# Optimization experiments

Measured on AMD Instinct MI355X. Metric: run time of the kernel, lower is better.

## Reference

```python
import jax, jax.numpy as jnp
import numpy as np

N_TH1 = 30
LB = 1e-20
UB = 1e20
LB_EXP = -20.0
UB_EXP = 20.0


def make_directions(n_th1):
    # Reproduces the TF __init__ direction sampling on the sphere.
    n_th2 = 2 * (n_th1 - 1) + 1
    th1 = np.linspace(-np.pi / 2, np.pi / 2, n_th1)
    th2 = np.linspace(-np.pi, np.pi, n_th2)
    c1, s1 = np.cos(th1), np.sin(th1)
    c2, s2 = np.cos(th2), np.sin(th2)
    dx = np.outer(c1[1:-1], c2[:-1])          # [n_th1-2, n_th2-1]
    dy = np.outer(c1[1:-1], s2[:-1])
    dz = np.broadcast_to(s1[1:-1, None], dx.shape)
    mid = np.stack([dx, dy, dz], -1).reshape(-1, 3)
    poles = np.array([[c1[0] * c2[0], c1[0] * s2[0], s1[0]],
                      [c1[-1] * c2[0], c1[-1] * s2[0], s1[-1]]])
    return np.concatenate([mid, poles], 0).astype(np.float32)  # [D, 3]


def setup_inputs() -> dict:
    key = jax.random.key(0)
    k1, k2, k3 = jax.random.split(key, 3)
    vertices = jax.random.normal(k1, (8, 64, 32, 3), jnp.float32)
    # smoothness is a p-norm exponent; realistic range [2, 20]
    smoothness = 2.0 + 18.0 * jax.random.uniform(k2, (8, 64), jnp.float32)
    pointcloud = jax.random.normal(k3, (8, 2048, 3), jnp.float32)
    return {"vertices": vertices, "smoothness": smoothness, "pointcloud": pointcloud}


def _spt_forward(vertices, smoothness):
    dirs = jnp.asarray(make_directions(N_TH1))            # [D, 3]
    B, P = vertices.shape[0], vertices.shape[1]
    mean_v = jnp.mean(vertices, axis=2, keepdims=True)    # [B,P,1,3]
    local_v = vertices - mean_v                           # [B,P,V,3]

    # z = <v, x> for every vertex/direction pair -> [B,P,V,D]
    z = jnp.einsum('bpvc,dc->bpvd', local_v, dirs)
    zm = jnp.maximum(z, 0.0)
    p = smoothness[:, :, None, None]                      # [B,P,1,1]

    # dynamic rescaling k = 10^ceil(...) to keep zm^p in fp range
    zm_max = jnp.max(zm, axis=2, keepdims=True)           # [B,P,1,D]
    zm_log = jnp.log(zm_max) / jnp.log(10.0)              # = max over V of log10(zm)
    exponent = zm_log * p
    lk = jnp.where(exponent < LB_EXP, (-15.0 - exponent) / p, 0.0)
    k = 10.0 ** jnp.clip(jnp.ceil(lk), 0.0, UB_EXP)       # [B,P,1,D]
    k = jax.lax.stop_gradient(k)                          # ceil has zero grad anyway

    zm = zm * k
    pos = zm > 0
    # clip(zm^p, lb, ub) - (zm==0)*lb  ==  where(zm>0, clip(zm^p,lb,ub), 0)
    zm_p = jnp.where(pos, jnp.clip(jnp.where(pos, zm, 1.0) ** p, LB, UB), 0.0)
    sum_zm_p = jnp.sum(zm_p, axis=2, keepdims=True)       # [B,P,1,D]
    spos = sum_zm_p > 0
    h = jnp.where(spos, jnp.clip(jnp.where(spos, sum_zm_p, 1.0) ** (1.0 / p), LB, UB), LB)

    # dh/dz = clip((zm/h)^(p-1), lb, ub)
    ratio = zm / h                                        # [B,P,V,D]
    rpos = ratio > 0
    dhdz = jnp.where(rpos, jnp.clip(jnp.where(rpos, ratio, 1.0) ** (p - 1.0), LB, UB), LB)
    # dh/dx = dhdz^T @ vertices -> surface points
    dhdx = jnp.einsum('bpvd,bpvc->bpdc', dhdz, local_v)   # [B,P,D,3]
    surf = dhdx + mean_v                                  # broadcast [B,P,1,3]

    h_out = jnp.clip(h / k, -UB, UB)                      # [B,P,1,D]
    h_out = jnp.transpose(h_out, (0, 1, 3, 2))            # [B,P,D,1]
    local_dirs = jnp.broadcast_to(dirs[None, None], (B, P) + dirs.shape)
    direction_h = jnp.concatenate([local_dirs, h_out], axis=-1)  # [B,P,D,4]
    points = surf.reshape(B, -1, 3)                       # [B, P*D, 3]
    mean_out = mean_v.reshape(B, P, 3)
    return points, direction_h, mean_out, local_v


def reference(vertices, smoothness, pointcloud):
    points, direction_h, mean_out, local_v = _spt_forward(vertices, smoothness)
    B, P = vertices.shape[0], vertices.shape[1]
    # overlap / retraction loops are truncated in the source; placeholders
    overlap = jnp.zeros((B, P, 1), jnp.float32)
    retraction = jnp.zeros((B, P, 1), jnp.float32)
    return (points, direction_h, overlap, retraction, mean_out, local_v)
```

## Files before the change

kernel.cpp:

```cpp
#include <hip/hip_runtime.h>
#include <math.h>

#define NBP 512
#define VV 32
#define DD 1626
#define TILE 256
#define NTILES 7

#define O_POINTS 0
#define O_DIRH   2497536
#define O_OVER   5827584
#define O_RETR   5828096
#define O_MEAN   5828608
#define O_LOCAL  5830144

#define L10_2 0.3010299956639812f
#define L2_10 3.321928094887362f
#define LH_MIN -66.43856189774725f

__device__ __forceinline__ float fexp2(float x) {
  return __builtin_amdgcn_exp2f(x);
}

__device__ __forceinline__ void make_dir(int d, float& x, float& y, float& z) {
  if (d < 1624) {
    int i1 = d / 58;
    int i2 = d - i1 * 58;
    i1 += 1;
    const float STEP = 0.10833078115826873f;
    float th1 = -1.5707963267948966f + (float)i1 * STEP;
    float th2 = -3.14159265358979323846f + (float)i2 * STEP;
    float s1, c1, s2, c2;
    sincosf(th1, &s1, &c1);
    sincosf(th2, &s2, &c2);
    x = c1 * c2; y = c1 * s2; z = s1;
  } else if (d == 1624) {
    x = -6.123234e-17f; y = -7.49880e-33f; z = -1.0f;
  } else {
    x = -6.123234e-17f; y = -7.49880e-33f; z = 1.0f;
  }
}

__global__ __launch_bounds__(256) void dirs_kernel(float* __restrict__ gdirs) {
  int d = blockIdx.x * 256 + threadIdx.x;
  if (d >= DD) return;
  float x, y, z;
  make_dir(d, x, y, z);
  gdirs[d * 3 + 0] = x;
  gdirs[d * 3 + 1] = y;
  gdirs[d * 3 + 2] = z;
}

__global__ __launch_bounds__(256) void spt_kernel(
    const float* __restrict__ vertices,
    const float* __restrict__ smooth,
    const float* __restrict__ gdirs,
    float* __restrict__ out)
{
  const int bp    = blockIdx.x;
  const int tile  = blockIdx.y;
  const int tid   = threadIdx.x;

  __shared__ float vb[VV * 3];
  __shared__ __align__(16) float slvx[VV];
  __shared__ __align__(16) float slvy[VV];
  __shared__ __align__(16) float slvz[VV];
  __shared__ float meanv[3];
  __shared__ __align__(16) float4 sdir[TILE];

  if (tid < VV * 3) vb[tid] = vertices[bp * (VV * 3) + tid];

  const int dbase = tile * TILE;
  const int dend  = (DD - dbase) < TILE ? (DD - dbase) : TILE;

  if (tid < dend) {
    const float* g = gdirs + (size_t)(dbase + tid) * 3;
    sdir[tid] = make_float4(g[0], g[1], g[2], 0.f);
  }
  __syncthreads();

  if (tid < 3) {
    float s = 0.f;
#pragma unroll
    for (int v = 0; v < VV; v++) s += vb[v * 3 + tid];
    meanv[tid] = s * (1.0f / 32.0f);
  }
  __syncthreads();
  if (tid < VV) {
    slvx[tid] = vb[tid * 3 + 0] - meanv[0];
    slvy[tid] = vb[tid * 3 + 1] - meanv[1];
    slvz[tid] = vb[tid * 3 + 2] - meanv[2];
  }
  __syncthreads();

  if (tile == 0) {
    if (tid < VV * 3) out[O_LOCAL + bp * (VV * 3) + tid] = vb[tid] - meanv[tid % 3];
    if (tid < 3)      out[O_MEAN + bp * 3 + tid] = meanv[tid];
    if (tid == 3)     out[O_OVER + bp] = 0.f;
    if (tid == 4)     out[O_RETR + bp] = 0.f;
  }

  if (tid >= dend) return;

  const float p     = smooth[bp];
  const float inv_p = 1.0f / p;
  const float pm1   = p - 1.0f;
  const float mx = meanv[0], my = meanv[1], mz = meanv[2];

  float4 dv = sdir[tid];
  const float dx = dv.x, dy = dv.y, dz = dv.z;
  const int d = dbase + tid;

  const float4* lvx4 = (const float4*)slvx;
  const float4* lvy4 = (const float4*)slvy;
  const float4* lvz4 = (const float4*)slvz;

  float lz[VV];
  float lmax = -INFINITY;
#pragma unroll
  for (int j = 0; j < VV / 4; j++) {
    float4 X = lvx4[j], Y = lvy4[j], Z = lvz4[j];
    float z0 = fmaxf(fmaf(X.x, dx, fmaf(Y.x, dy, Z.x * dz)), 0.f);
    float z1 = fmaxf(fmaf(X.y, dx, fmaf(Y.y, dy, Z.y * dz)), 0.f);
    float z2 = fmaxf(fmaf(X.z, dx, fmaf(Y.z, dy, Z.z * dz)), 0.f);
    float z3 = fmaxf(fmaf(X.w, dx, fmaf(Y.w, dy, Z.w * dz)), 0.f);
    float l0 = __log2f(z0), l1 = __log2f(z1);
    float l2 = __log2f(z2), l3 = __log2f(z3);
    lz[j * 4 + 0] = l0; lz[j * 4 + 1] = l1;
    lz[j * 4 + 2] = l2; lz[j * 4 + 3] = l3;
    lmax = fmaxf(lmax, fmaxf(fmaxf(l0, l1), fmaxf(l2, l3)));
  }

  const float expo = lmax * (p * L10_2);
  float kc = 0.f;
  if (expo < -20.f) {
    kc = fminf(fmaxf(ceilf((-15.f - expo) * inv_p), 0.f), 20.f);
  }
  const float kcl = kc * L2_10;
  const float pkc = p * kcl;

  float s0 = 0.f, s1 = 0.f, s2 = 0.f, s3 = 0.f;
#pragma unroll
  for (int j = 0; j < VV / 4; j++) {
    s0 += fminf(fexp2(fmaf(p, lz[j * 4 + 0], pkc)), 1e20f);
    s1 += fminf(fexp2(fmaf(p, lz[j * 4 + 1], pkc)), 1e20f);
    s2 += fminf(fexp2(fmaf(p, lz[j * 4 + 2], pkc)), 1e20f);
    s3 += fminf(fexp2(fmaf(p, lz[j * 4 + 3], pkc)), 1e20f);
  }
  const float ssum = (s0 + s1) + (s2 + s3);

  float lh = LH_MIN;
  if (ssum > 0.f) lh = inv_p * __log2f(ssum);

  const float c3 = pm1 * (kcl - lh);
  float ax = 0.f, ay = 0.f, az = 0.f;
#pragma unroll
  for (int j = 0; j < VV / 4; j++) {
    float4 X = lvx4[j], Y = lvy4[j], Z = lvz4[j];
    float d0 = fminf(fexp2(fmaf(pm1, lz[j * 4 + 0], c3)), 1e20f);
    float d1 = fminf(fexp2(fmaf(pm1, lz[j * 4 + 1], c3)), 1e20f);
    float d2 = fminf(fexp2(fmaf(pm1, lz[j * 4 + 2], c3)), 1e20f);
    float d3 = fminf(fexp2(fmaf(pm1, lz[j * 4 + 3], c3)), 1e20f);
    ax = fmaf(d0, X.x, fmaf(d1, X.y, fmaf(d2, X.z, fmaf(d3, X.w, ax))));
    ay = fmaf(d0, Y.x, fmaf(d1, Y.y, fmaf(d2, Y.z, fmaf(d3, Y.w, ay))));
    az = fmaf(d0, Z.x, fmaf(d1, Z.y, fmaf(d2, Z.z, fmaf(d3, Z.w, az))));
  }

  const int pbase = bp * DD + d;
  out[O_POINTS + pbase * 3 + 0] = ax + mx;
  out[O_POINTS + pbase * 3 + 1] = ay + my;
  out[O_POINTS + pbase * 3 + 2] = az + mz;

  dv.w = fexp2(lh - kcl);
  ((float4*)(out + O_DIRH))[pbase] = dv;
}

extern "C" void kernel_launch(void* const* d_in, const int* in_sizes, int n_in,
                              void* d_out, int out_size, void* d_ws, size_t ws_size,
                              hipStream_t stream) {
  const float* vertices = (const float*)d_in[0];
  const float* smooth   = (const float*)d_in[1];
  float* out = (float*)d_out;
  float* gdirs = (float*)d_ws;

  dirs_kernel<<<dim3((DD + 255) / 256), 256, 0, stream>>>(gdirs);
  spt_kernel<<<dim3(NBP, NTILES), 256, 0, stream>>>(vertices, smooth, gdirs, out);
}
```

Before: 80.51 us.

## Process each half of the directions per block with a wave-shuffle mean reduction

The grid changes from 7 direction tiles of 256 per point set to 2 halves of 813 directions, and each thread now handles up to 4 directions in sequence. Directions are stored as float4 in the workspace and loaded straight into registers instead of being staged through shared memory. The per-set mean is computed with a wave shuffle reduction rather than a serial shared-memory loop, which drops two barriers. This amortises setup work per direction and removes the wasted threads in the partial last tile, but it also reduces the number of blocks and adds register pressure under launch_bounds(256,4).

```diff
diff --git a/kernel.cpp b/kernel.cpp
--- a/kernel.cpp
+++ b/kernel.cpp
@@ -4,8 +4,7 @@
 #define NBP 512
 #define VV 32
 #define DD 1626
-#define TILE 256
-#define NTILES 7
+#define DHALF 813
 
 #define O_POINTS 0
 #define O_DIRH   2497536
@@ -41,138 +40,150 @@
   }
 }
 
-__global__ __launch_bounds__(256) void dirs_kernel(float* __restrict__ gdirs) {
+__global__ __launch_bounds__(256) void dirs_kernel(float4* __restrict__ gdirs) {
   int d = blockIdx.x * 256 + threadIdx.x;
   if (d >= DD) return;
   float x, y, z;
   make_dir(d, x, y, z);
-  gdirs[d * 3 + 0] = x;
-  gdirs[d * 3 + 1] = y;
-  gdirs[d * 3 + 2] = z;
+  gdirs[d] = make_float4(x, y, z, 0.f);
 }
 
-__global__ __launch_bounds__(256) void spt_kernel(
+__global__ __launch_bounds__(256, 4) void spt_kernel(
     const float* __restrict__ vertices,
     const float* __restrict__ smooth,
-    const float* __restrict__ gdirs,
+    const float4* __restrict__ gdirs,
     float* __restrict__ out)
 {
-  const int bp    = blockIdx.x;
-  const int tile  = blockIdx.y;
-  const int tid   = threadIdx.x;
+  const int bp   = blockIdx.x;
+  const int tile = blockIdx.y;
+  const int tid  = threadIdx.x;
 
-  __shared__ float vb[VV * 3];
   __shared__ __align__(16) float slvx[VV];
   __shared__ __align__(16) float slvy[VV];
   __shared__ __align__(16) float slvz[VV];
-  __shared__ float meanv[3];
-  __shared__ __align__(16) float4 sdir[TILE];
 
-  if (tid < VV * 3) vb[tid] = vertices[bp * (VV * 3) + tid];
+  const int dbase = tile * DHALF;
 
-  const int dbase = tile * TILE;
-  const int dend  = (DD - dbase) < TILE ? (DD - dbase) : TILE;
+  float4 dir4[4];
+#pragma unroll
+  for (int i = 0; i < 4; i++) {
+    int idx = i * 256 + tid;
+    idx = idx < DHALF ? idx : (DHALF - 1);
+    dir4[i] = gdirs[dbase + idx];
+  }
 
-  if (tid < dend) {
-    const float* g = gdirs + (size_t)(dbase + tid) * 3;
-    sdir[tid] = make_float4(g[0], g[1], g[2], 0.f);
+  const int v = tid & 31;
+  const float* vp = vertices + bp * (VV * 3) + v * 3;
+  const float vx = vp[0], vy = vp[1], vz = vp[2];
+  float sx = vx, sy = vy, sz = vz;
+#pragma unroll
+  for (int m = 16; m >= 1; m >>= 1) {
+    sx += __shfl_xor(sx, m);
+    sy += __shfl_xor(sy, m);
+    sz += __shfl_xor(sz, m);
   }
-  __syncthreads();
-
-  if (tid < 3) {
-    float s = 0.f;
-#pragma unroll
-    for (int v = 0; v < VV; v++) s += vb[v * 3 + tid];
-    meanv[tid] = s * (1.0f / 32.0f);
-  }
-  __syncthreads();
+  const float mx = sx * (1.0f / 32.0f);
+  const float my = sy * (1.0f / 32.0f);
+  const float mz = sz * (1.0f / 32.0f);
   if (tid < VV) {
-    slvx[tid] = vb[tid * 3 + 0] - meanv[0];
-    slvy[tid] = vb[tid * 3 + 1] - meanv[1];
-    slvz[tid] = vb[tid * 3 + 2] - meanv[2];
+    slvx[tid] = vx - mx;
+    slvy[tid] = vy - my;
+    slvz[tid] = vz - mz;
   }
   __syncthreads();
 
   if (tile == 0) {
-    if (tid < VV * 3) out[O_LOCAL + bp * (VV * 3) + tid] = vb[tid] - meanv[tid % 3];
-    if (tid < 3)      out[O_MEAN + bp * 3 + tid] = meanv[tid];
-    if (tid == 3)     out[O_OVER + bp] = 0.f;
-    if (tid == 4)     out[O_RETR + bp] = 0.f;
+    if (tid < VV * 3) {
+      const int vv = tid / 3, c = tid - vv * 3;
+      const float val = (c == 0) ? slvx[vv] : ((c == 1) ? slvy[vv] : slvz[vv]);
+      out[O_LOCAL + bp * (VV * 3) + tid] = val;
+    }
+    if (tid == 0) {
+      out[O_MEAN + bp * 3 + 0] = mx;
+      out[O_MEAN + bp * 3 + 1] = my;
+      out[O_MEAN + bp * 3 + 2] = mz;
+      out[O_OVER + bp] = 0.f;
+      out[O_RETR + bp] = 0.f;
+    }
   }
-
-  if (tid >= dend) return;
 
   const float p     = smooth[bp];
   const float inv_p = 1.0f / p;
   const float pm1   = p - 1.0f;
-  const float mx = meanv[0], my = meanv[1], mz = meanv[2];
-
-  float4 dv = sdir[tid];
-  const float dx = dv.x, dy = dv.y, dz = dv.z;
-  const int d = dbase + tid;
+  const float plt   = p * L10_2;
 
   const float4* lvx4 = (const float4*)slvx;
   const float4* lvy4 = (const float4*)slvy;
   const float4* lvz4 = (const float4*)slvz;
 
-  float lz[VV];
-  float lmax = -INFINITY;
+  auto process = [&](int idx, float4 dv) {
+    const int d = dbase + idx;
+    const float dx = dv.x, dy = dv.y, dz = dv.z;
+
+    float lz[VV];
+    float lmax = -INFINITY;
 #pragma unroll
-  for (int j = 0; j < VV / 4; j++) {
-    float4 X = lvx4[j], Y = lvy4[j], Z = lvz4[j];
-    float z0 = fmaxf(fmaf(X.x, dx, fmaf(Y.x, dy, Z.x * dz)), 0.f);
-    float z1 = fmaxf(fmaf(X.y, dx, fmaf(Y.y, dy, Z.y * dz)), 0.f);
-    float z2 = fmaxf(fmaf(X.z, dx, fmaf(Y.z, dy, Z.z * dz)), 0.f);
-    float z3 = fmaxf(fmaf(X.w, dx, fmaf(Y.w, dy, Z.w * dz)), 0.f);
-    float l0 = __log2f(z0), l1 = __log2f(z1);
-    float l2 = __log2f(z2), l3 = __log2f(z3);
-    lz[j * 4 + 0] = l0; lz[j * 4 + 1] = l1;
-    lz[j * 4 + 2] = l2; lz[j * 4 + 3] = l3;
-    lmax = fmaxf(lmax, fmaxf(fmaxf(l0, l1), fmaxf(l2, l3)));
-  }
+    for (int j = 0; j < VV / 4; j++) {
+      float4 X = lvx4[j], Y = lvy4[j], Z = lvz4[j];
+      float z0 = fmaxf(fmaf(X.x, dx, fmaf(Y.x, dy, Z.x * dz)), 0.f);
+      float z1 = fmaxf(fmaf(X.y, dx, fmaf(Y.y, dy, Z.y * dz)), 0.f);
+      float z2 = fmaxf(fmaf(X.z, dx, fmaf(Y.z, dy, Z.z * dz)), 0.f);
+      float z3 = fmaxf(fmaf(X.w, dx, fmaf(Y.w, dy, Z.w * dz)), 0.f);
+      float l0 = __log2f(z0), l1 = __log2f(z1);
+      float l2 = __log2f(z2), l3 = __log2f(z3);
+      lz[j * 4 + 0] = l0; lz[j * 4 + 1] = l1;
+      lz[j * 4 + 2] = l2; lz[j * 4 + 3] = l3;
+      lmax = fmaxf(lmax, fmaxf(fmaxf(l0, l1), fmaxf(l2, l3)));
+    }
 
-  const float expo = lmax * (p * L10_2);
-  float kc = 0.f;
-  if (expo < -20.f) {
-    kc = fminf(fmaxf(ceilf((-15.f - expo) * inv_p), 0.f), 20.f);
-  }
-  const float kcl = kc * L2_10;
-  const float pkc = p * kcl;
+    const float expo = lmax * plt;
+    float kc = 0.f;
+    if (expo < -20.f) {
+      kc = fminf(fmaxf(ceilf((-15.f - expo) * inv_p), 0.f), 20.f);
+    }
+    const float kcl = kc * L2_10;
+    const float pkc = p * kcl;
 
-  float s0 = 0.f, s1 = 0.f, s2 = 0.f, s3 = 0.f;
+    float s0 = 0.f, s1 = 0.f, s2 = 0.f, s3 = 0.f;
 #pragma unroll
-  for (int j = 0; j < VV / 4; j++) {
-    s0 += fminf(fexp2(fmaf(p, lz[j * 4 + 0], pkc)), 1e20f);
-    s1 += fminf(fexp2(fmaf(p, lz[j * 4 + 1], pkc)), 1e20f);
-    s2 += fminf(fexp2(fmaf(p, lz[j * 4 + 2], pkc)), 1e20f);
-    s3 += fminf(fexp2(fmaf(p, lz[j * 4 + 3], pkc)), 1e20f);
-  }
-  const float ssum = (s0 + s1) + (s2 + s3);
+    for (int j = 0; j < VV / 4; j++) {
+      s0 += fminf(fexp2(fmaf(p, lz[j * 4 + 0], pkc)), 1e20f);
+      s1 += fminf(fexp2(fmaf(p, lz[j * 4 + 1], pkc)), 1e20f);
+      s2 += fminf(fexp2(fmaf(p, lz[j * 4 + 2], pkc)), 1e20f);
+      s3 += fminf(fexp2(fmaf(p, lz[j * 4 + 3], pkc)), 1e20f);
+    }
+    const float ssum = (s0 + s1) + (s2 + s3);
 
-  float lh = LH_MIN;
-  if (ssum > 0.f) lh = inv_p * __log2f(ssum);
+    float lh = LH_MIN;
+    if (ssum > 0.f) lh = inv_p * __log2f(ssum);
 
-  const float c3 = pm1 * (kcl - lh);
-  float ax = 0.f, ay = 0.f, az = 0.f;
+    const float c3 = pm1 * (kcl - lh);
+    float ax = 0.f, ay = 0.f, az = 0.f;
 #pragma unroll
-  for (int j = 0; j < VV / 4; j++) {
-    float4 X = lvx4[j], Y = lvy4[j], Z = lvz4[j];
-    float d0 = fminf(fexp2(fmaf(pm1, lz[j * 4 + 0], c3)), 1e20f);
-    float d1 = fminf(fexp2(fmaf(pm1, lz[j * 4 + 1], c3)), 1e20f);
-    float d2 = fminf(fexp2(fmaf(pm1, lz[j * 4 + 2], c3)), 1e20f);
-    float d3 = fminf(fexp2(fmaf(pm1, lz[j * 4 + 3], c3)), 1e20f);
-    ax = fmaf(d0, X.x, fmaf(d1, X.y, fmaf(d2, X.z, fmaf(d3, X.w, ax))));
-    ay = fmaf(d0, Y.x, fmaf(d1, Y.y, fmaf(d2, Y.z, fmaf(d3, Y.w, ay))));
-    az = fmaf(d0, Z.x, fmaf(d1, Z.y, fmaf(d2, Z.z, fmaf(d3, Z.w, az))));
-  }
+    for (int j = 0; j < VV / 4; j++) {
+      float4 X = lvx4[j], Y = lvy4[j], Z = lvz4[j];
+      float d0 = fminf(fexp2(fmaf(pm1, lz[j * 4 + 0], c3)), 1e20f);
+      float d1 = fminf(fexp2(fmaf(pm1, lz[j * 4 + 1], c3)), 1e20f);
+      float d2 = fminf(fexp2(fmaf(pm1, lz[j * 4 + 2], c3)), 1e20f);
+      float d3 = fminf(fexp2(fmaf(pm1, lz[j * 4 + 3], c3)), 1e20f);
+      ax = fmaf(d0, X.x, fmaf(d1, X.y, fmaf(d2, X.z, fmaf(d3, X.w, ax))));
+      ay = fmaf(d0, Y.x, fmaf(d1, Y.y, fmaf(d2, Y.z, fmaf(d3, Y.w, ay))));
+      az = fmaf(d0, Z.x, fmaf(d1, Z.y, fmaf(d2, Z.z, fmaf(d3, Z.w, az))));
+    }
 
-  const int pbase = bp * DD + d;
-  out[O_POINTS + pbase * 3 + 0] = ax + mx;
-  out[O_POINTS + pbase * 3 + 1] = ay + my;
-  out[O_POINTS + pbase * 3 + 2] = az + mz;
+    const int pbase = bp * DD + d;
+    out[O_POINTS + pbase * 3 + 0] = ax + mx;
+    out[O_POINTS + pbase * 3 + 1] = ay + my;
+    out[O_POINTS + pbase * 3 + 2] = az + mz;
 
-  dv.w = fexp2(lh - kcl);
-  ((float4*)(out + O_DIRH))[pbase] = dv;
+    dv.w = fexp2(lh - kcl);
+    ((float4*)(out + O_DIRH))[pbase] = dv;
+  };
+
+  process(tid,        dir4[0]);
+  process(256 + tid,  dir4[1]);
+  process(512 + tid,  dir4[2]);
+  if (tid < DHALF - 768) process(768 + tid, dir4[3]);
 }
 
 extern "C" void kernel_launch(void* const* d_in, const int* in_sizes, int n_in,
@@ -181,8 +192,8 @@
   const float* vertices = (const float*)d_in[0];
   const float* smooth   = (const float*)d_in[1];
   float* out = (float*)d_out;
-  float* gdirs = (float*)d_ws;
+  float4* gdirs = (float4*)d_ws;
 
   dirs_kernel<<<dim3((DD + 255) / 256), 256, 0, stream>>>(gdirs);
-  spt_kernel<<<dim3(NBP, NTILES), 256, 0, stream>>>(vertices, smooth, gdirs, out);
+  spt_kernel<<<dim3(NBP, 2), 256, 0, stream>>>(vertices, smooth, gdirs, out);
 }
```

After: 111.8 us. +38.9%, slower.
